# Performance work log

Measured on AMD Instinct MI355X. Metric: run time of the kernel, lower is better.

The kernel has to match this reference:

```python
import jax, jax.numpy as jnp
import numpy as np

N_TOTAL_USERS = 200000
N_TOTAL_ITEMS = 300000
N_DOM_USERS = 60000
N_DOM_ITEMS = 90000
N_DOMAINS = 3
DIM = 32           # hidden_dim // 2
N_LAYERS = 2
ALPHA = 0.1


def grec_conv(src, dst, x, n_nodes):
    """LightGCN-style propagation with APPNP residual (alpha), symmetric norm.
    Edge dropout is disabled (eval mode). x: [n_nodes, d]."""
    ones = jnp.ones(src.shape[0], dtype=x.dtype)
    deg = jax.ops.segment_sum(ones, dst, num_segments=n_nodes)
    inv_sqrt = jax.lax.rsqrt(jnp.maximum(deg, 1.0))
    w = inv_sqrt[src] * inv_sqrt[dst]            # [E] edge norm
    h = x
    for _ in range(N_LAYERS):
        msg = h[src] * w[:, None]                # gather + scale, [E, d]
        agg = jax.ops.segment_sum(msg, dst, num_segments=n_nodes)
        h = (1.0 - ALPHA) * agg + ALPHA * x      # residual to layer-0 emb
    return h


def setup_inputs() -> dict:
    key = jax.random.key(0)
    ks = jax.random.split(key, 8)
    return {
        "dom_edges": jax.random.randint(ks[0], (2, 2000000), 0, N_DOM_USERS + N_DOM_ITEMS, dtype=jnp.int32),
        "sep_edges": jax.random.randint(ks[1], (3, 2, 2000000), 0, N_TOTAL_USERS + N_TOTAL_ITEMS, dtype=jnp.int32),
        "aggr_user_w": 0.1 * jax.random.normal(ks[2], (N_TOTAL_USERS, DIM), dtype=jnp.float32),
        "aggr_item_w": 0.1 * jax.random.normal(ks[3], (N_TOTAL_ITEMS, DIM), dtype=jnp.float32),
        "dom_user_w": 0.1 * jax.random.normal(ks[4], (N_DOM_USERS, DIM), dtype=jnp.float32),
        "dom_item_w": 0.1 * jax.random.normal(ks[5], (N_DOM_ITEMS, DIM), dtype=jnp.float32),
        "user_ids_dom": jnp.arange(N_DOM_USERS, dtype=jnp.int32),
        "item_ids_dom": jnp.arange(N_DOM_ITEMS, dtype=jnp.int32),
        "users": jax.random.randint(ks[6], (8192,), 0, N_DOM_USERS).astype(jnp.int64),
        "items": jax.random.randint(ks[7], (8192,), 0, N_DOM_ITEMS).astype(jnp.int64),
    }


def reference(dom_edges, sep_edges, aggr_user_w, aggr_item_w,
              dom_user_w, dom_item_w, user_ids_dom, item_ids_dom,
              users, items):
    n_dom_nodes = N_DOM_USERS + N_DOM_ITEMS
    n_all_nodes = N_TOTAL_USERS + N_TOTAL_ITEMS

    # ---- intra-domain conv (mode='dis_intra') on the domain graph ----
    x_intra = jnp.concatenate([dom_user_w, dom_item_w], axis=0)
    h_intra = grec_conv(dom_edges[0], dom_edges[1], x_intra, n_dom_nodes)
    user_intra = h_intra[:N_DOM_USERS]
    item_intra = h_intra[N_DOM_USERS:]

    # ---- inter-domain conv (mode='dis_inter'): per-domain sep graphs, mean ----
    x_inter = jnp.concatenate([aggr_user_w, aggr_item_w], axis=0)
    embs = []
    for d in range(N_DOMAINS):  # small fixed loop over domains
        h = grec_conv(sep_edges[d, 0], sep_edges[d, 1], x_inter, n_all_nodes)
        uss = h[:N_TOTAL_USERS][user_ids_dom]   # gather this domain's users
        its = h[N_TOTAL_USERS:][item_ids_dom]   # gather this domain's items
        embs.append(jnp.concatenate([uss, its], axis=0))
    light_out = jnp.mean(jnp.stack(embs, axis=1), axis=1)  # [n_dom_nodes, DIM]
    user_inter = light_out[:N_DOM_USERS]
    item_inter = light_out[N_DOM_USERS:]

    # ---- concat inter || intra, score query pairs ----
    all_users = jnp.concatenate([user_inter, user_intra], axis=1)  # [Nu_d, 64]
    all_items = jnp.concatenate([item_inter, item_intra], axis=1)
    users_emb = all_users[users]
    items_emb = all_items[items]
    gamma = jnp.sum(users_emb * items_emb, axis=1)  # [B]
    return gamma
```

## Files before the change

### kernel.cpp

```cpp
#include <hip/hip_runtime.h>


static constexpr int NTU = 200000, NTI = 300000, NDU = 60000, NDI = 90000;
static constexpr int NDOMN = 150000, NALLN = 500000, NE = 2000000;
static constexpr int DIM = 32, NQ = 8192;
static constexpr int TN = NDOMN + 3 * NALLN;

static constexpr int BSH_I = 9,  BN_I = 512,  NBK_I = 293, CAP_I = 7680;
static constexpr int BSH_E = 11, BN_E = 2048, NBK_E = 245, CAP_E = 9216;
static constexpr int GEW_I = NBK_I * CAP_I;
static constexpr int GEW_E = NBK_E * CAP_E;
static constexpr int GEW   = GEW_I + 3 * GEW_E;
static constexpr int NBCK  = NBK_I + 3 * NBK_E;
static constexpr int ACT_CAP = 360000;
static constexpr int PCHUNK = 4096;
static constexpr int PBLK_PG = (NE + PCHUNK - 1) / PCHUNK;
static constexpr int PUNROLL = PCHUNK / 256;

static constexpr size_t a256(size_t x) { return (x + 255) & ~(size_t)255; }
static constexpr size_t O_NEED  = 0;
static constexpr size_t O_N1    = a256((size_t)NDOMN * 4);
static constexpr size_t ZB      = O_N1 + a256(TN);
static constexpr size_t O_RANK  = ZB;
static constexpr size_t O_BSUM  = O_RANK + a256((size_t)NDOMN * 4);
static constexpr size_t O_BCUR  = O_BSUM + 1024;
static constexpr size_t O_DEG8  = O_BCUR + a256(NBCK * 4);
static constexpr size_t O_OFF   = O_DEG8 + a256(TN);
static constexpr size_t O_RANK1 = O_OFF  + a256((size_t)TN * 4);
static constexpr size_t O_ALIST = O_RANK1 + a256((size_t)TN * 4);
static constexpr size_t O_NLIST = O_ALIST + a256((size_t)ACT_CAP * 4);
static constexpr size_t O_GE    = O_NLIST + a256((size_t)16384 * 4);
static constexpr size_t O_AGG1  = O_GE   + (size_t)GEW * 4;
static constexpr size_t O_A2    = O_AGG1 + (size_t)ACT_CAP * DIM * 4;

__global__ void k_setup(uint4* __restrict__ zp, int n16, unsigned* __restrict__ bcur) {
    int t = blockIdx.x * blockDim.x + threadIdx.x;
    if (t < n16) zp[t] = make_uint4(0u, 0u, 0u, 0u);
    if (t < NBCK) {
        int g, b;
        if (t < NBK_I) { g = 0; b = t; }
        else { int r = t - NBK_I; g = 1 + r / NBK_E; b = r - (g - 1) * NBK_E; }
        unsigned geb = (g == 0) ? 0u : (unsigned)(GEW_I + (g - 1) * GEW_E);
        unsigned cap = (g == 0) ? CAP_I : CAP_E;
        bcur[t] = geb + (unsigned)b * cap;
    }
}

__global__ void k_scatter_needed(const int* __restrict__ users, const int* __restrict__ items,
                                 unsigned* __restrict__ need) {
    int t = blockIdx.x * blockDim.x + threadIdx.x;
    if (t < NQ)            need[users[t]] = 1u;
    else if (t < 2 * NQ)   need[NDU + items[t - NQ]] = 1u;
}

__global__ __launch_bounds__(256, 5) void k_part(const int* __restrict__ dom, const int* __restrict__ sep,
                                                 const unsigned* __restrict__ need,
                                                 unsigned char* __restrict__ n1,
                                                 unsigned* __restrict__ bcur,
                                                 unsigned* __restrict__ gE) {
    __shared__ unsigned sortedE[PCHUNK];
    __shared__ unsigned short sortedB[PCHUNK];
    __shared__ unsigned hist[512], lstart[512], gbase[512];
    __shared__ unsigned wsum[4];
    int t = threadIdx.x;
    int g = blockIdx.x / PBLK_PG;
    int chunk = blockIdx.x - g * PBLK_PG;
    const int* src = (g == 0) ? dom : sep + (size_t)(g - 1) * 2 * NE;
    const int* dst = src + NE;
    int bsh = (g == 0) ? BSH_I : BSH_E;
    unsigned bnm = (g == 0) ? (BN_I - 1) : (BN_E - 1);
    int nbk = (g == 0) ? NBK_I : NBK_E;
    unsigned cap = (g == 0) ? CAP_I : CAP_E;
    unsigned geb = (g == 0) ? 0u : (unsigned)(GEW_I + (g - 1) * GEW_E);
    int bco = (g == 0) ? 0 : NBK_I + (g - 1) * NBK_E;
    unsigned char* n1g = n1 + ((g == 0) ? 0 : (NDOMN + (size_t)(g - 1) * NALLN));
    hist[t] = 0u; hist[t + 256] = 0u;
    __syncthreads();
    int base = chunk * PCHUNK;
    unsigned pk[PUNROLL]; unsigned short bb[PUNROLL];
    #pragma unroll
    for (int i = 0; i < PUNROLL; i++) {
        int idx = base + i * 256 + t;
        if (idx < NE) {
            unsigned s = (unsigned)src[idx], d = (unsigned)dst[idx];
            unsigned nd;
            if (g == 0) nd = need[d];
            else nd = (d < NDU) ? need[d] : ((d >= NTU && d < NTU + NDI) ? need[NDU + d - NTU] : 0u);
            if (nd) n1g[s] = 1;
            unsigned b = d >> bsh;
            pk[i] = ((d & bnm) << 19) | s;
            bb[i] = (unsigned short)b;
            atomicAdd(&hist[b], 1u);
        } else bb[i] = 0xFFFF;
    }
    __syncthreads();
    unsigned c0 = hist[2 * t], c1 = hist[2 * t + 1], ps = c0 + c1;
    int lane = t & 63, wid = t >> 6;
    unsigned x = ps;
    #pragma unroll
    for (int o = 1; o < 64; o <<= 1) {
        unsigned y = __shfl_up(x, o);
        if (lane >= o) x += y;
    }
    if (lane == 63) wsum[wid] = x;
    __syncthreads();
    unsigned wo = 0;
    if (wid > 0) wo += wsum[0];
    if (wid > 1) wo += wsum[1];
    if (wid > 2) wo += wsum[2];
    x += wo;
    unsigned total = wsum[0] + wsum[1] + wsum[2] + wsum[3];
    unsigned e0 = x - ps, e1 = e0 + c0;
    lstart[2 * t] = e0; lstart[2 * t + 1] = e1;
    hist[2 * t] = e0; hist[2 * t + 1] = e1;
    if (2 * t < nbk && c0) {
        unsigned gb = atomicAdd(&bcur[bco + 2 * t], c0);
        gbase[2 * t] = (gb + c0 <= geb + (unsigned)(2 * t + 1) * cap) ? gb : 0xFFFFFFFFu;
    }
    if (2 * t + 1 < nbk && c1) {
        unsigned gb = atomicAdd(&bcur[bco + 2 * t + 1], c1);
        gbase[2 * t + 1] = (gb + c1 <= geb + (unsigned)(2 * t + 2) * cap) ? gb : 0xFFFFFFFFu;
    }
    __syncthreads();
    #pragma unroll
    for (int i = 0; i < PUNROLL; i++) {
        if (bb[i] != 0xFFFF) {
            unsigned p = atomicAdd(&hist[bb[i]], 1u);
            sortedE[p] = pk[i]; sortedB[p] = bb[i];
        }
    }
    __syncthreads();
    for (unsigned idx = t; idx < total; idx += 256) {
        unsigned b = sortedB[idx], gb = gbase[b];
        if (gb != 0xFFFFFFFFu) gE[gb + (idx - lstart[b])] = sortedE[idx];
    }
}

__global__ __launch_bounds__(256) void k_sortb(unsigned* __restrict__ gE,
                                               const unsigned* __restrict__ bcur,
                                               unsigned* __restrict__ off,
                                               unsigned char* __restrict__ deg8) {
    __shared__ unsigned ed[CAP_E];
    __shared__ unsigned h2[BN_E];
    __shared__ unsigned scanarr[256];
    int t = threadIdx.x, bx = blockIdx.x;
    int g, b;
    if (bx < NBK_I) { g = 0; b = bx; }
    else { int r = bx - NBK_I; g = 1 + r / NBK_E; b = r - (g - 1) * NBK_E; }
    int bn = (g == 0) ? BN_I : BN_E;
    unsigned cap = (g == 0) ? CAP_I : CAP_E;
    unsigned geb = (g == 0) ? 0u : (unsigned)(GEW_I + (g - 1) * GEW_E);
    int bco = (g == 0) ? 0 : NBK_I + (g - 1) * NBK_E;
    int nb = (g == 0) ? 0 : NDOMN + (g - 1) * NALLN;
    int nnodes = (g == 0) ? NDOMN : NALLN;
    unsigned j0 = geb + (unsigned)b * cap;
    unsigned cnt = bcur[bco + b] - j0;
    if (cnt > cap) cnt = cap;
    for (unsigned j = t; j < cnt; j += 256) ed[j] = gE[j0 + j];
    for (int k = t; k < bn; k += 256) h2[k] = 0u;
    __syncthreads();
    for (unsigned j = t; j < cnt; j += 256) atomicAdd(&h2[ed[j] >> 19], 1u);
    __syncthreads();
    int E = bn >> 8;
    unsigned c[8], pre[8]; unsigned ssum = 0;
    int k0 = t * E;
    for (int q = 0; q < E; q++) { c[q] = h2[k0 + q]; pre[q] = ssum; ssum += c[q]; }
    scanarr[t] = ssum;
    unsigned x = ssum;
    for (int o = 1; o < 256; o <<= 1) {
        __syncthreads();
        unsigned y = (t >= o) ? scanarr[t - o] : 0u;
        __syncthreads();
        x += y; scanarr[t] = x;
    }
    __syncthreads();
    unsigned excl = x - ssum;
    int vb = b * bn;
    for (int q = 0; q < E; q++) {
        int v = vb + k0 + q;
        if (v < nnodes) { off[nb + v] = j0 + excl + pre[q]; deg8[nb + v] = (unsigned char)c[q]; }
    }
    for (int q = 0; q < E; q++) h2[k0 + q] = excl + pre[q];
    __syncthreads();
    for (unsigned j = t; j < cnt; j += 256) {
        unsigned e = ed[j];
        unsigned p = atomicAdd(&h2[e >> 19], 1u);
        gE[j0 + p] = e & 0x7FFFFu;
    }
}

static constexpr int SCAN_T = 256;

template <int EL, typename T>
__global__ void k_scan1(const T* __restrict__ in, unsigned* __restrict__ out,
                        unsigned* __restrict__ bsum, int n) {
    __shared__ unsigned lds[SCAN_T];
    int b = blockIdx.x, t = threadIdx.x;
    int base = b * (SCAN_T * EL) + t * EL;
    unsigned v[EL]; unsigned s = 0;
    for (int i = 0; i < EL; i++) { int idx = base + i; v[i] = (idx < n) ? (unsigned)in[idx] : 0u; s += v[i]; }
    lds[t] = s;
    unsigned x = s;
    for (int o = 1; o < SCAN_T; o <<= 1) {
        __syncthreads();
        unsigned y = (t >= o) ? lds[t - o] : 0u;
        __syncthreads();
        x += y; lds[t] = x;
    }
    unsigned running = x - s;
    for (int i = 0; i < EL; i++) { int idx = base + i; if (idx < n) out[idx] = running; running += v[i]; }
    if (t == SCAN_T - 1) bsum[b] = x;
}

__global__ void k_scan2(unsigned* __restrict__ bsum, int nbv) {
    __shared__ unsigned lds[SCAN_T];
    int t = threadIdx.x;
    unsigned s = (t < nbv) ? bsum[t] : 0u;
    lds[t] = s;
    unsigned x = s;
    for (int o = 1; o < SCAN_T; o <<= 1) {
        __syncthreads();
        unsigned y = (t >= o) ? lds[t - o] : 0u;
        __syncthreads();
        x += y; lds[t] = x;
    }
    if (t < nbv) bsum[t] = x - s;
}

template <int CH>
__global__ void k_scan3(unsigned* __restrict__ out, const unsigned* __restrict__ bsum, int n) {
    int i = blockIdx.x * blockDim.x + threadIdx.x;
    if (i < n) out[i] += bsum[i / CH];
}

__global__ void k_lists(const unsigned char* __restrict__ n1, const unsigned* __restrict__ rank1,
                        unsigned* __restrict__ alist,
                        const unsigned* __restrict__ need, const unsigned* __restrict__ rank,
                        unsigned* __restrict__ nlist) {
    int t = blockIdx.x * blockDim.x + threadIdx.x;
    if (t < TN && n1[t]) { unsigned r = rank1[t]; if (r < ACT_CAP) alist[r] = (unsigned)t; }
    if (t < NDOMN && need[t]) nlist[rank[t]] = (unsigned)t;
}

__global__ void k_gather1(const unsigned* __restrict__ alist, const unsigned* __restrict__ off,
                          const unsigned char* __restrict__ deg8, const unsigned* __restrict__ gE,
                          const float* __restrict__ auw, const float* __restrict__ aiw,
                          const float* __restrict__ duw, const float* __restrict__ diw,
                          float* __restrict__ agg1) {
    int t = blockIdx.x * blockDim.x + threadIdx.x;
    int r = t >> 3, c = t & 7;
    if (r >= ACT_CAP) return;
    unsigned gv = alist[r];
    if (gv >= (unsigned)TN) return;
    int g, nb;
    if ((int)gv < NDOMN) { g = 0; nb = 0; }
    else { int q = (int)gv - NDOMN; g = 1 + q / NALLN; nb = NDOMN + (g - 1) * NALLN; }
    int v = (int)gv - nb;
    const float* uw = g ? auw : duw;
    const float* iw = g ? aiw : diw;
    int UB = g ? NTU : NDU;
    const unsigned char* d8 = deg8 + nb;
    unsigned j0 = off[gv];
    int dg = deg8[gv];
    float invd = rsqrtf(fmaxf((float)dg, 1.0f));
    float4 acc = make_float4(0.f, 0.f, 0.f, 0.f);
    int j = 0;
    for (; j + 4 <= dg; j += 4) {
        int s0 = (int)gE[j0 + j], s1 = (int)gE[j0 + j + 1];
        int s2 = (int)gE[j0 + j + 2], s3 = (int)gE[j0 + j + 3];
        float4 x0 = ((const float4*)((s0 < UB) ? uw + (size_t)s0 * DIM : iw + (size_t)(s0 - UB) * DIM))[c];
        float4 x1 = ((const float4*)((s1 < UB) ? uw + (size_t)s1 * DIM : iw + (size_t)(s1 - UB) * DIM))[c];
        float4 x2 = ((const float4*)((s2 < UB) ? uw + (size_t)s2 * DIM : iw + (size_t)(s2 - UB) * DIM))[c];
        float4 x3 = ((const float4*)((s3 < UB) ? uw + (size_t)s3 * DIM : iw + (size_t)(s3 - UB) * DIM))[c];
        float w0 = rsqrtf(fmaxf((float)d8[s0], 1.0f)) * invd;
        float w1 = rsqrtf(fmaxf((float)d8[s1], 1.0f)) * invd;
        float w2 = rsqrtf(fmaxf((float)d8[s2], 1.0f)) * invd;
        float w3 = rsqrtf(fmaxf((float)d8[s3], 1.0f)) * invd;
        acc.x += w0 * x0.x + w1 * x1.x + w2 * x2.x + w3 * x3.x;
        acc.y += w0 * x0.y + w1 * x1.y + w2 * x2.y + w3 * x3.y;
        acc.z += w0 * x0.z + w1 * x1.z + w2 * x2.z + w3 * x3.z;
        acc.w += w0 * x0.w + w1 * x1.w + w2 * x2.w + w3 * x3.w;
    }
    for (; j < dg; j++) {
        int s = (int)gE[j0 + j];
        float w = rsqrtf(fmaxf((float)d8[s], 1.0f)) * invd;
        float4 xv = ((const float4*)((s < UB) ? uw + (size_t)s * DIM : iw + (size_t)(s - UB) * DIM))[c];
        acc.x += w * xv.x; acc.y += w * xv.y; acc.z += w * xv.z; acc.w += w * xv.w;
    }
    float4 xo = ((const float4*)((v < UB) ? uw + (size_t)v * DIM : iw + (size_t)(v - UB) * DIM))[c];
    float4 A;
    A.x = 0.9f * acc.x + 0.1f * xo.x;
    A.y = 0.9f * acc.y + 0.1f * xo.y;
    A.z = 0.9f * acc.z + 0.1f * xo.z;
    A.w = 0.9f * acc.w + 0.1f * xo.w;
    ((float4*)(agg1 + (size_t)r * DIM))[c] = A;
}

__global__ void k_gather2(const unsigned* __restrict__ nlist, const unsigned* __restrict__ rank,
                          const unsigned* __restrict__ rank1, const unsigned* __restrict__ off,
                          const unsigned char* __restrict__ deg8, const unsigned* __restrict__ gE,
                          const float* __restrict__ agg1, float* __restrict__ a2) {
    int t = blockIdx.x * blockDim.x + threadIdx.x;
    int idx = t >> 3, c = t & 7;
    int g = idx >> 14;
    int r = idx & 16383;
    unsigned v = nlist[r];
    if (v >= (unsigned)NDOMN) return;
    int nb, node;
    if (g == 0) { nb = 0; node = (int)v; }
    else { nb = NDOMN + (g - 1) * NALLN; node = ((int)v < NDU) ? (int)v : NTU + ((int)v - NDU); }
    int gv = nb + node;
    unsigned j0 = off[gv];
    int dg = deg8[gv];
    float invd = rsqrtf(fmaxf((float)dg, 1.0f));
    const unsigned char* d8 = deg8 + nb;
    const unsigned* r1 = rank1 + nb;
    float4 acc = make_float4(0.f, 0.f, 0.f, 0.f);
    int j = 0;
    for (; j + 4 <= dg; j += 4) {
        int s0 = (int)gE[j0 + j], s1 = (int)gE[j0 + j + 1];
        int s2 = (int)gE[j0 + j + 2], s3 = (int)gE[j0 + j + 3];
        unsigned a0 = r1[s0], a1 = r1[s1], a2i = r1[s2], a3 = r1[s3];
        float4 A0 = ((const float4*)(agg1 + (size_t)a0 * DIM))[c];
        float4 A1 = ((const float4*)(agg1 + (size_t)a1 * DIM))[c];
        float4 A2 = ((const float4*)(agg1 + (size_t)a2i * DIM))[c];
        float4 A3 = ((const float4*)(agg1 + (size_t)a3 * DIM))[c];
        float w0 = rsqrtf(fmaxf((float)d8[s0], 1.0f)) * invd;
        float w1 = rsqrtf(fmaxf((float)d8[s1], 1.0f)) * invd;
        float w2 = rsqrtf(fmaxf((float)d8[s2], 1.0f)) * invd;
        float w3 = rsqrtf(fmaxf((float)d8[s3], 1.0f)) * invd;
        acc.x += w0 * A0.x + w1 * A1.x + w2 * A2.x + w3 * A3.x;
        acc.y += w0 * A0.y + w1 * A1.y + w2 * A2.y + w3 * A3.y;
        acc.z += w0 * A0.z + w1 * A1.z + w2 * A2.z + w3 * A3.z;
        acc.w += w0 * A0.w + w1 * A1.w + w2 * A2.w + w3 * A3.w;
    }
    for (; j < dg; j++) {
        int s = (int)gE[j0 + j];
        unsigned ar = r1[s];
        float w = rsqrtf(fmaxf((float)d8[s], 1.0f)) * invd;
        float4 A = ((const float4*)(agg1 + (size_t)ar * DIM))[c];
        acc.x += w * A.x; acc.y += w * A.y; acc.z += w * A.z; acc.w += w * A.w;
    }
    ((float4*)(a2 + ((size_t)g * 16384 + rank[v]) * DIM))[c] = acc;
}

__global__ void k_gamma(const int* __restrict__ users, const int* __restrict__ items,
                        const unsigned* __restrict__ rank, const float* __restrict__ a2,
                        const float* __restrict__ auw, const float* __restrict__ aiw,
                        const float* __restrict__ duw, const float* __restrict__ diw,
                        float* __restrict__ out) {
    int t = blockIdx.x * blockDim.x + threadIdx.x;
    int q = t >> 3;
    if (q >= NQ) return;
    int c = t & 7;
    int u = users[q], it = items[q];
    int ru = (int)rank[u], ri = (int)rank[NDU + it];
    auto A2 = [&](int g, int r) { return ((const float4*)(a2 + ((size_t)g * 16384 + r) * DIM))[c]; };
    float4 Du = A2(0, ru), Di = A2(0, ri);
    float4 U1 = A2(1, ru), U2 = A2(2, ru), U3 = A2(3, ru);
    float4 V1 = A2(1, ri), V2 = A2(2, ri), V3 = A2(3, ri);
    float4 xu = ((const float4*)(auw + (size_t)u * DIM))[c];
    float4 xi = ((const float4*)(aiw + (size_t)it * DIM))[c];
    float4 yu = ((const float4*)(duw + (size_t)u * DIM))[c];
    float4 yi = ((const float4*)(diw + (size_t)it * DIM))[c];
    float s = 0.f;
    s += (0.3f * (U1.x + U2.x + U3.x) + 0.1f * xu.x) * (0.3f * (V1.x + V2.x + V3.x) + 0.1f * xi.x);
    s += (0.3f * (U1.y + U2.y + U3.y) + 0.1f * xu.y) * (0.3f * (V1.y + V2.y + V3.y) + 0.1f * xi.y);
    s += (0.3f * (U1.z + U2.z + U3.z) + 0.1f * xu.z) * (0.3f * (V1.z + V2.z + V3.z) + 0.1f * xi.z);
    s += (0.3f * (U1.w + U2.w + U3.w) + 0.1f * xu.w) * (0.3f * (V1.w + V2.w + V3.w) + 0.1f * xi.w);
    s += (0.9f * Du.x + 0.1f * yu.x) * (0.9f * Di.x + 0.1f * yi.x);
    s += (0.9f * Du.y + 0.1f * yu.y) * (0.9f * Di.y + 0.1f * yi.y);
    s += (0.9f * Du.z + 0.1f * yu.z) * (0.9f * Di.z + 0.1f * yi.z);
    s += (0.9f * Du.w + 0.1f * yu.w) * (0.9f * Di.w + 0.1f * yi.w);
    s += __shfl_xor(s, 1);
    s += __shfl_xor(s, 2);
    s += __shfl_xor(s, 4);
    if (c == 0) out[q] = s;
}

extern "C" void kernel_launch(void* const* d_in, const int* in_sizes, int n_in,
                              void* d_out, int out_size, void* d_ws, size_t ws_size,
                              hipStream_t stream) {
    const int*   dom_edges = (const int*)d_in[0];
    const int*   sep_edges = (const int*)d_in[1];
    const float* auw       = (const float*)d_in[2];
    const float* aiw       = (const float*)d_in[3];
    const float* duw       = (const float*)d_in[4];
    const float* diw       = (const float*)d_in[5];
    const int*   users     = (const int*)d_in[8];
    const int*   items     = (const int*)d_in[9];
    float*       out       = (float*)d_out;

    char* ws = (char*)d_ws;
    unsigned*      need  = (unsigned*)(ws + O_NEED);
    unsigned char* n1    = (unsigned char*)(ws + O_N1);
    unsigned*      rank  = (unsigned*)(ws + O_RANK);
    unsigned*      bsum  = (unsigned*)(ws + O_BSUM);
    unsigned*      bcur  = (unsigned*)(ws + O_BCUR);
    unsigned char* deg8  = (unsigned char*)(ws + O_DEG8);
    unsigned*      off   = (unsigned*)(ws + O_OFF);
    unsigned*      rank1 = (unsigned*)(ws + O_RANK1);
    unsigned*      alist = (unsigned*)(ws + O_ALIST);
    unsigned*      nlist = (unsigned*)(ws + O_NLIST);
    unsigned*      gE    = (unsigned*)(ws + O_GE);
    float*         agg1  = (float*)(ws + O_AGG1);
    float*         a2    = (float*)(ws + O_A2);

    const int BLK = 256;
    auto cdiv = [](long a, long b) { return (int)((a + b - 1) / b); };

    int n16 = (int)(ZB / 16);
    k_setup<<<cdiv(n16, BLK), BLK, 0, stream>>>((uint4*)ws, n16, bcur);
    k_scatter_needed<<<cdiv(2 * NQ, BLK), BLK, 0, stream>>>(users, items, need);

    {
        int nbv = cdiv(NDOMN, SCAN_T * 8);
        k_scan1<8, unsigned><<<nbv, SCAN_T, 0, stream>>>(need, rank, bsum, NDOMN);
        k_scan2<<<1, SCAN_T, 0, stream>>>(bsum, nbv);
        k_scan3<SCAN_T * 8><<<cdiv(NDOMN, BLK), BLK, 0, stream>>>(rank, bsum, NDOMN);
    }

    k_part<<<4 * PBLK_PG, 256, 0, stream>>>(dom_edges, sep_edges, need, n1, bcur, gE);

    k_sortb<<<NBCK, 256, 0, stream>>>(gE, bcur, off, deg8);

    {
        int nbv = cdiv(TN, SCAN_T * 32);
        k_scan1<32, unsigned char><<<nbv, SCAN_T, 0, stream>>>(n1, rank1, bsum, TN);
        k_scan2<<<1, SCAN_T, 0, stream>>>(bsum, nbv);
        k_scan3<SCAN_T * 32><<<cdiv(TN, BLK), BLK, 0, stream>>>(rank1, bsum, TN);
    }

    k_lists<<<cdiv(TN, BLK), BLK, 0, stream>>>(n1, rank1, alist, need, rank, nlist);

    k_gather1<<<cdiv((long)ACT_CAP * 8, BLK), BLK, 0, stream>>>(alist, off, deg8, gE,
                                                                auw, aiw, duw, diw, agg1);
    k_gather2<<<cdiv((long)4 * 16384 * 8, BLK), BLK, 0, stream>>>(nlist, rank, rank1, off, deg8,
                                                                  gE, agg1, a2);

    k_gamma<<<cdiv((long)NQ * 8, BLK), BLK, 0, stream>>>(users, items, rank, a2,
                                                         auw, aiw, duw, diw, out);
}
```

Measured before the change: 410.9 us.

## Move needed-source marking out of partition into CSR-based marking kernel

```diff
diff --git a/kernel.cpp b/kernel.cpp
--- a/kernel.cpp
+++ b/kernel.cpp
@@ -15,7 +15,6 @@
 static constexpr int ACT_CAP = 360000;
 static constexpr int PCHUNK = 4096;
 static constexpr int PBLK_PG = (NE + PCHUNK - 1) / PCHUNK;
-static constexpr int PUNROLL = PCHUNK / 256;
 
 static constexpr size_t a256(size_t x) { return (x + 255) & ~(size_t)255; }
 static constexpr size_t O_NEED  = 0;
@@ -53,13 +52,9 @@
     else if (t < 2 * NQ)   need[NDU + items[t - NQ]] = 1u;
 }
 
-__global__ __launch_bounds__(256, 5) void k_part(const int* __restrict__ dom, const int* __restrict__ sep,
-                                                 const unsigned* __restrict__ need,
-                                                 unsigned char* __restrict__ n1,
+__global__ __launch_bounds__(256, 6) void k_part(const int* __restrict__ dom, const int* __restrict__ sep,
                                                  unsigned* __restrict__ bcur,
                                                  unsigned* __restrict__ gE) {
-    __shared__ unsigned sortedE[PCHUNK];
-    __shared__ unsigned short sortedB[PCHUNK];
     __shared__ unsigned hist[512], lstart[512], gbase[512];
     __shared__ unsigned wsum[4];
     int t = threadIdx.x;
@@ -73,25 +68,30 @@
     unsigned cap = (g == 0) ? CAP_I : CAP_E;
     unsigned geb = (g == 0) ? 0u : (unsigned)(GEW_I + (g - 1) * GEW_E);
     int bco = (g == 0) ? 0 : NBK_I + (g - 1) * NBK_E;
-    unsigned char* n1g = n1 + ((g == 0) ? 0 : (NDOMN + (size_t)(g - 1) * NALLN));
     hist[t] = 0u; hist[t + 256] = 0u;
     __syncthreads();
-    int base = chunk * PCHUNK;
-    unsigned pk[PUNROLL]; unsigned short bb[PUNROLL];
+    int vbase = chunk * (PCHUNK / 4);
+    unsigned pk[16]; unsigned short bb[16];
     #pragma unroll
-    for (int i = 0; i < PUNROLL; i++) {
-        int idx = base + i * 256 + t;
-        if (idx < NE) {
-            unsigned s = (unsigned)src[idx], d = (unsigned)dst[idx];
-            unsigned nd;
-            if (g == 0) nd = need[d];
-            else nd = (d < NDU) ? need[d] : ((d >= NTU && d < NTU + NDI) ? need[NDU + d - NTU] : 0u);
-            if (nd) n1g[s] = 1;
-            unsigned b = d >> bsh;
-            pk[i] = ((d & bnm) << 19) | s;
-            bb[i] = (unsigned short)b;
-            atomicAdd(&hist[b], 1u);
-        } else bb[i] = 0xFFFF;
+    for (int i = 0; i < 4; i++) {
+        int vi = vbase + i * 256 + t;
+        if (vi < NE / 4) {
+            int4 sv = ((const int4*)src)[vi];
+            int4 dv = ((const int4*)dst)[vi];
+            int ss[4] = {sv.x, sv.y, sv.z, sv.w};
+            int dd[4] = {dv.x, dv.y, dv.z, dv.w};
+            #pragma unroll
+            for (int e = 0; e < 4; e++) {
+                unsigned d = (unsigned)dd[e];
+                unsigned b = d >> bsh;
+                pk[i * 4 + e] = ((d & bnm) << 19) | (unsigned)ss[e];
+                bb[i * 4 + e] = (unsigned short)b;
+                atomicAdd(&hist[b], 1u);
+            }
+        } else {
+            #pragma unroll
+            for (int e = 0; e < 4; e++) bb[i * 4 + e] = 0xFFFF;
+        }
     }
     __syncthreads();
     unsigned c0 = hist[2 * t], c1 = hist[2 * t + 1], ps = c0 + c1;
@@ -109,7 +109,6 @@
     if (wid > 1) wo += wsum[1];
     if (wid > 2) wo += wsum[2];
     x += wo;
-    unsigned total = wsum[0] + wsum[1] + wsum[2] + wsum[3];
     unsigned e0 = x - ps, e1 = e0 + c0;
     lstart[2 * t] = e0; lstart[2 * t + 1] = e1;
     hist[2 * t] = e0; hist[2 * t + 1] = e1;
@@ -123,16 +122,13 @@
     }
     __syncthreads();
     #pragma unroll
-    for (int i = 0; i < PUNROLL; i++) {
+    for (int i = 0; i < 16; i++) {
         if (bb[i] != 0xFFFF) {
-            unsigned p = atomicAdd(&hist[bb[i]], 1u);
-            sortedE[p] = pk[i]; sortedB[p] = bb[i];
+            unsigned b = bb[i];
+            unsigned p = atomicAdd(&hist[b], 1u);
+            unsigned gb = gbase[b];
+            if (gb != 0xFFFFFFFFu) gE[gb + (p - lstart[b])] = pk[i];
         }
-    }
-    __syncthreads();
-    for (unsigned idx = t; idx < total; idx += 256) {
-        unsigned b = sortedB[idx], gb = gbase[b];
-        if (gb != 0xFFFFFFFFu) gE[gb + (idx - lstart[b])] = sortedE[idx];
     }
 }
 
@@ -187,6 +183,23 @@
         unsigned p = atomicAdd(&h2[e >> 19], 1u);
         gE[j0 + p] = e & 0x7FFFFu;
     }
+}
+
+__global__ void k_mark(const unsigned* __restrict__ need, const unsigned* __restrict__ off,
+                       const unsigned char* __restrict__ deg8, const unsigned* __restrict__ gE,
+                       unsigned char* __restrict__ n1) {
+    int t = blockIdx.x * blockDim.x + threadIdx.x;
+    if (t >= 4 * NDOMN) return;
+    int v = t >> 2, g = t & 3;
+    if (!need[v]) return;
+    int nb, node;
+    if (g == 0) { nb = 0; node = v; }
+    else { nb = NDOMN + (g - 1) * NALLN; node = (v < NDU) ? v : NTU + (v - NDU); }
+    int gv = nb + node;
+    unsigned j0 = off[gv];
+    int dg = deg8[gv];
+    unsigned char* n1g = n1 + nb;
+    for (int j = 0; j < dg; j++) n1g[gE[j0 + j]] = 1;
 }
 
 static constexpr int SCAN_T = 256;
@@ -420,9 +433,11 @@
         k_scan3<SCAN_T * 8><<<cdiv(NDOMN, BLK), BLK, 0, stream>>>(rank, bsum, NDOMN);
     }
 
-    k_part<<<4 * PBLK_PG, 256, 0, stream>>>(dom_edges, sep_edges, need, n1, bcur, gE);
+    k_part<<<4 * PBLK_PG, 256, 0, stream>>>(dom_edges, sep_edges, bcur, gE);
 
     k_sortb<<<NBCK, 256, 0, stream>>>(gE, bcur, off, deg8);
+
+    k_mark<<<cdiv((long)4 * NDOMN, BLK), BLK, 0, stream>>>(need, off, deg8, gE, n1);
 
     {
         int nbv = cdiv(TN, SCAN_T * 32);
```

Result: no change. 403.5 us (-1.8%).
